# Kernel tuning notes

Measured on AMD Instinct MI355X. Metric: run time of the kernel, lower is better.

Reference implementation:

```python
import jax, jax.numpy as jnp
import numpy as np

D_MODEL = 1024
N_HEADS = 16
DK = D_MODEL // N_HEADS


def setup_inputs() -> dict:
    key = jax.random.key(0)
    k1, k2, k3, k4 = jax.random.split(key, 4)
    x = jax.random.normal(k1, (2, 2048, D_MODEL), dtype=jnp.float32)
    # torch nn.Linear stores weight as [out_features, in_features]
    W_qkv = jax.random.normal(k2, (3 * D_MODEL, D_MODEL), dtype=jnp.float32) * (1.0 / np.sqrt(D_MODEL))
    W_proj = jax.random.normal(k3, (D_MODEL, D_MODEL), dtype=jnp.float32) * (1.0 / np.sqrt(D_MODEL))
    b_proj = jax.random.normal(k4, (D_MODEL,), dtype=jnp.float32) * 0.01
    return {"x": x, "W_qkv": W_qkv, "W_proj": W_proj, "b_proj": b_proj}


def reference(x, W_qkv, W_proj, b_proj):
    B, L, D = x.shape
    qkv = x @ W_qkv.T                      # [B, L, 3D]
    q, k, v = jnp.split(qkv, 3, axis=-1)   # each [B, L, D]

    def split_heads(t):
        return t.reshape(B, L, N_HEADS, DK).transpose(0, 2, 1, 3)  # [B, H, L, dk]

    q, k, v = map(split_heads, (q, k, v))
    scale = jnp.float32(1.0 / np.sqrt(DK))
    scores = jnp.einsum('bhid,bhjd->bhij', q, k) * scale  # [B, H, L, L]
    attn = jax.nn.softmax(scores, axis=-1)
    out = jnp.einsum('bhij,bhjd->bhid', attn, v)           # [B, H, L, dk]
    out = out.transpose(0, 2, 1, 3).reshape(B, L, D)
    return out @ W_proj.T + b_proj
```

## Files before the change

kernel.cpp:

```cpp
#include <hip/hip_runtime.h>
#include <stdint.h>

typedef unsigned short ushort_t;
typedef __bf16 bf16x4 __attribute__((ext_vector_type(4)));
typedef __bf16 bf16x8 __attribute__((ext_vector_type(8)));
typedef float f32x4 __attribute__((ext_vector_type(4)));
typedef float f32x16 __attribute__((ext_vector_type(16)));
typedef unsigned short us8 __attribute__((ext_vector_type(8)));
typedef unsigned short us4v __attribute__((ext_vector_type(4)));

__device__ __forceinline__ float bf2f(ushort_t u) {
  union { uint32_t u; float f; } v; v.u = ((uint32_t)u) << 16; return v.f;
}
__device__ __forceinline__ ushort_t f2bf(float f) {
  union { float f; uint32_t u; } v; v.f = f;
  uint32_t u = v.u;
  uint32_t r = (u + 0x7FFFu + ((u >> 16) & 1u)) >> 16;
  return (ushort_t)r;
}
__device__ __forceinline__ uint32_t pkbf(float a, float b) {
  __bf16 x = (__bf16)a, y = (__bf16)b;
  uint32_t ux = __builtin_bit_cast(unsigned short, x);
  uint32_t uy = __builtin_bit_cast(unsigned short, y);
  return ux | (uy << 16);
}
__device__ __forceinline__ void gload_lds16(const void* g, void* l) {
  __builtin_amdgcn_global_load_lds(
      (const __attribute__((address_space(1))) void*)g,
      (__attribute__((address_space(3))) void*)l, 16, 0, 0);
}
__device__ __forceinline__ void tr2(const ushort_t* p, bf16x4& lo, bf16x4& hi) {
  asm volatile("ds_read_b64_tr_b16 %0, %2\n\t"
               "ds_read_b64_tr_b16 %1, %2 offset:128"
               : "=&v"(lo), "=&v"(hi)
               : "v"((const __attribute__((address_space(3))) ushort_t*)p));
}

template <typename T> __device__ __forceinline__ T to_out(float f);
template <> __device__ __forceinline__ ushort_t to_out<ushort_t>(float f) { return f2bf(f); }
template <> __device__ __forceinline__ float to_out<float>(float f) { return f; }

#define SCQ 0.1803368801111204f

__global__ void f2b3_kernel(const float* __restrict__ a, ushort_t* __restrict__ ao,
                            const float* __restrict__ b, ushort_t* __restrict__ bo,
                            const float* __restrict__ c, ushort_t* __restrict__ co) {
  int blk = blockIdx.x;
  const float* src; ushort_t* dst; int n4, b0, nb;
  if (blk < 1024)      { src = a; dst = ao; n4 = 1048576; b0 = blk;        nb = 1024; }
  else if (blk < 1792) { src = b; dst = bo; n4 = 786432;  b0 = blk - 1024; nb = 768; }
  else                 { src = c; dst = co; n4 = 262144;  b0 = blk - 1792; nb = 256; }
  for (int i = b0 * 256 + threadIdx.x; i < n4; i += nb * 256) {
    float4 v = ((const float4*)src)[i];
    us4v o;
    o[0] = f2bf(v.x); o[1] = f2bf(v.y); o[2] = f2bf(v.z); o[3] = f2bf(v.w);
    ((us4v*)dst)[i] = o;
  }
}

template<bool BIAS, typename OT, bool SCALEQ, bool MERGEA>
__global__ __launch_bounds__(256, 2) void gemm_bt(
    const ushort_t* __restrict__ A, const ushort_t* __restrict__ W,
    const float* __restrict__ bias, OT* __restrict__ C,
    int M, int N, int K,
    const ushort_t* __restrict__ A2, const float* __restrict__ lb)
{
  __shared__ ushort_t As[128 * 64];
  __shared__ ushort_t Bs[128 * 64];
  const int t = threadIdx.x;
  const int w = t >> 6, lane = t & 63;
  const int lg = lane >> 4, lc = lane & 15;
  const int rowbase = blockIdx.y * 128;
  const int colbase = blockIdx.x * 128;
  const int wr = (w >> 1) * 64, wc = (w & 1) * 64;

  f32x4 acc[4][4] = {};
  const int nkt = K >> 6;

  for (int kt = 0; kt < nkt; ++kt) {
#pragma unroll
    for (int i = 0; i < 4; ++i) {
      int off = (i * 256 + t) * 16;
      int row = off >> 7;
      int cb  = off & 127;
      int ec  = cb ^ ((row & 7) << 4);
      if constexpr (MERGEA) {
        int drow = rowbase + row;
        int kcol = kt * 64 + (cb >> 1);
        us8 v1 = *(const us8*)(A  + (size_t)drow * K + kcol);
        us8 v2 = *(const us8*)(A2 + (size_t)drow * K + kcol);
        float inv = 1.f / (lb[(size_t)drow * 16 + (kcol >> 6)] +
                           lb[65536 + (size_t)drow * 16 + (kcol >> 6)]);
        us8 o;
#pragma unroll
        for (int j = 0; j < 8; ++j)
          o[j] = f2bf((bf2f(v1[j]) + bf2f(v2[j])) * inv);
        *(us8*)((char*)As + (off ^ ((row & 7) << 4))) = o;
      } else {
        gload_lds16(A + (size_t)(rowbase + row) * K + kt * 64 + (ec >> 1),
                    (char*)As + off);
      }
      gload_lds16(W + (size_t)(colbase + row) * K + kt * 64 + (ec >> 1),
                  (char*)Bs + off);
    }
    __syncthreads();
#pragma unroll
    for (int kk = 0; kk < 2; ++kk) {
      bf16x8 af[4], bf[4];
#pragma unroll
      for (int m = 0; m < 4; ++m) {
        int row = wr + m * 16 + lc;
        int kb  = (lg * 16 + kk * 64) ^ ((row & 7) << 4);
        af[m] = *(const bf16x8*)((const char*)As + row * 128 + kb);
        int col = wc + m * 16 + lc;
        int kb2 = (lg * 16 + kk * 64) ^ ((col & 7) << 4);
        bf[m] = *(const bf16x8*)((const char*)Bs + col * 128 + kb2);
      }
#pragma unroll
      for (int m = 0; m < 4; ++m)
#pragma unroll
        for (int n = 0; n < 4; ++n)
          acc[m][n] = __builtin_amdgcn_mfma_f32_16x16x32_bf16(af[m], bf[n],
                                                              acc[m][n], 0, 0, 0);
    }
    __syncthreads();
  }

#pragma unroll
  for (int m = 0; m < 4; ++m) {
    int r0 = rowbase + wr + m * 16 + lg * 4;
#pragma unroll
    for (int n = 0; n < 4; ++n) {
      int c0 = colbase + wc + n * 16 + lc;
      float bv = 0.f;
      if (BIAS) bv = bias[c0];
      float qs = 1.f;
      if (SCALEQ) qs = (c0 < 1024) ? SCQ : 1.f;
#pragma unroll
      for (int j = 0; j < 4; ++j)
        C[(size_t)(r0 + j) * N + c0] = to_out<OT>(acc[m][n][j] * qs + bv);
    }
  }
}

__global__ __launch_bounds__(512, 4) void attn_fwd(
    const ushort_t* __restrict__ qkv, ushort_t* __restrict__ o1,
    ushort_t* __restrict__ o2, float* __restrict__ lbuf)
{
  __shared__ ushort_t Ks[2][64 * 64];
  __shared__ ushort_t Vs[2][64 * 64];

  const int t = threadIdx.x, w = t >> 6, lane = t & 63;
  const int l31 = lane & 31, hi = lane >> 5;
  const int lc = lane & 15;

  const int d = blockIdx.x;
  const int qt = (d >> 3) & 7;
  const int bhs = (d & 7) * 8 + (d >> 6);
  const int bh = bhs >> 1, split = bhs & 1;
  const int b = bh >> 4, h = bh & 15;

  const ushort_t* Qg = qkv + (size_t)(b * 2048) * 3072 + h * 64;
  const ushort_t* Kg = Qg + 1024 + (size_t)split * 1024 * 3072;
  const ushort_t* Vg = Qg + 2048 + (size_t)split * 1024 * 3072;

  auto stage_k = [&](ushort_t* Kd, int kt) {
    int off = t * 16;
    int row = off >> 7;
    int cb  = off & 127;
    int ec  = cb ^ ((row & 7) << 4);
    gload_lds16(Kg + (size_t)(kt * 64 + row) * 3072 + (ec >> 1),
                (char*)Kd + off);
  };
  const int vr  = t >> 3;
  const int vc0 = (t & 7) * 8;
  const int vdst = (vc0 >> 4) * 2048 + (vr >> 2) * 128 + (vr & 3) * 32 +
                   (vc0 & 8) * 2;

  const ushort_t* qrow_p = Qg + (size_t)(qt * 256 + w * 32 + l31) * 3072;
  bf16x8 qf[4];
#pragma unroll
  for (int kk = 0; kk < 4; ++kk)
    qf[kk] = *(const bf16x8*)(qrow_p + kk * 16 + hi * 8);

  stage_k(Ks[0], 0);
  {
    us8 v = *(const us8*)(Vg + (size_t)vr * 3072 + vc0);
    *(us8*)((char*)Vs[0] + vdst) = v;
  }
  __syncthreads();

  f32x16 oacc0 = {}, oacc1 = {};
  float l = 0.f;
  const int m16 = (lane >> 4) & 1;

  int cur = 0;
  for (int kt = 0; kt < 16; ++kt) {
    us8 vnext;
    if (kt < 15) {
      stage_k(Ks[cur ^ 1], kt + 1);
      vnext = *(const us8*)(Vg + (size_t)((kt + 1) * 64 + vr) * 3072 + vc0);
    }

    const ushort_t* Kc = Ks[cur];
    f32x16 s0 = {}, s1 = {};
    __builtin_amdgcn_s_setprio(1);
#pragma unroll
    for (int kk = 0; kk < 4; ++kk) {
      int cbyte = (kk * 32 + hi * 16);
      int r0 = l31, r1 = 32 + l31;
      bf16x8 kf0 = *(const bf16x8*)((const char*)Kc + r0 * 128 +
                                    (cbyte ^ ((r0 & 7) << 4)));
      bf16x8 kf1 = *(const bf16x8*)((const char*)Kc + r1 * 128 +
                                    (cbyte ^ ((r1 & 7) << 4)));
      s0 = __builtin_amdgcn_mfma_f32_32x32x16_bf16(kf0, qf[kk], s0, 0, 0, 0);
      s1 = __builtin_amdgcn_mfma_f32_32x32x16_bf16(kf1, qf[kk], s1, 0, 0, 0);
    }
    __builtin_amdgcn_s_setprio(0);

#pragma unroll
    for (int i = 0; i < 16; ++i) {
      s0[i] = __builtin_amdgcn_exp2f(s0[i]);
      s1[i] = __builtin_amdgcn_exp2f(s1[i]);
    }
    float rs = (((s0[0] + s0[1]) + (s0[2] + s0[3])) +
                ((s0[4] + s0[5]) + (s0[6] + s0[7]))) +
               (((s0[8] + s0[9]) + (s0[10] + s0[11])) +
                ((s0[12] + s0[13]) + (s0[14] + s0[15])));
    float rt = (((s1[0] + s1[1]) + (s1[2] + s1[3])) +
                ((s1[4] + s1[5]) + (s1[6] + s1[7]))) +
               (((s1[8] + s1[9]) + (s1[10] + s1[11])) +
                ((s1[12] + s1[13]) + (s1[14] + s1[15])));
    l += rs + rt;

    uint32_t pk0[8], pk1[8];
#pragma unroll
    for (int j = 0; j < 8; ++j) {
      pk0[j] = pkbf(s0[2 * j], s0[2 * j + 1]);
      pk1[j] = pkbf(s1[2 * j], s1[2 * j + 1]);
    }

    if (kt < 15)
      *(us8*)((char*)Vs[cur ^ 1] + vdst) = vnext;

    const ushort_t* Vc = Vs[cur];
    bf16x8 pa[4], vf[4][2];
#pragma unroll
    for (int ks = 0; ks < 4; ++ks) {
      int j0 = 4 * (ks & 1);
      uint32_t x0 = (ks < 2) ? pk0[j0]     : pk1[j0];
      uint32_t x1 = (ks < 2) ? pk0[j0 + 1] : pk1[j0 + 1];
      uint32_t y0 = (ks < 2) ? pk0[j0 + 2] : pk1[j0 + 2];
      uint32_t y1 = (ks < 2) ? pk0[j0 + 3] : pk1[j0 + 3];
      asm volatile("v_permlane32_swap_b32 %0, %1" : "+v"(x0), "+v"(y0));
      asm volatile("v_permlane32_swap_b32 %0, %1" : "+v"(x1), "+v"(y1));
      union { uint32_t du[4]; bf16x8 v; } U;
      U.du[0] = x0; U.du[1] = x1; U.du[2] = y0; U.du[3] = y1;
      pa[ks] = U.v;
#pragma unroll
      for (int nd = 0; nd < 2; ++nd) {
        bf16x4 lo, hh;
        tr2(Vc + (nd * 2 + m16) * 1024 + (4 * ks + 2 * hi) * 64 + lc * 4, lo, hh);
        vf[ks][nd] = __builtin_shufflevector(lo, hh, 0, 1, 2, 3, 4, 5, 6, 7);
      }
    }
    asm volatile("s_waitcnt lgkmcnt(0)" ::: "memory");
    __builtin_amdgcn_sched_barrier(0);
    __builtin_amdgcn_s_setprio(1);
#pragma unroll
    for (int ks = 0; ks < 4; ++ks) {
      oacc0 = __builtin_amdgcn_mfma_f32_32x32x16_bf16(pa[ks], vf[ks][0], oacc0, 0, 0, 0);
      oacc1 = __builtin_amdgcn_mfma_f32_32x32x16_bf16(pa[ks], vf[ks][1], oacc1, 0, 0, 0);
    }
    __builtin_amdgcn_s_setprio(0);

    __syncthreads();
    cur ^= 1;
  }

  l += __shfl_xor(l, 32);

  ushort_t* op = split ? o2 : o1;
#pragma unroll
  for (int r = 0; r < 16; ++r) {
    int crow = (r & 3) + 8 * (r >> 2) + 4 * hi;
    int qrow = qt * 256 + w * 32 + crow;
    size_t base = ((size_t)(b * 2048 + qrow)) * 1024 + h * 64 + l31;
    op[base]      = f2bf(oacc0[r]);
    op[base + 32] = f2bf(oacc1[r]);
  }
  if (hi == 0) {
    int qrow = qt * 256 + w * 32 + l31;
    lbuf[(size_t)split * 65536 + (size_t)(b * 2048 + qrow) * 16 + h] = l;
  }
}

extern "C" void kernel_launch(void* const* d_in, const int* in_sizes, int n_in,
                              void* d_out, int out_size, void* d_ws, size_t ws_size,
                              hipStream_t stream) {
  const float* x     = (const float*)d_in[0];
  const float* Wqkv  = (const float*)d_in[1];
  const float* Wproj = (const float*)d_in[2];
  const float* bproj = (const float*)d_in[3];
  float* out = (float*)d_out;

  ushort_t* qkv   = (ushort_t*)d_ws;
  ushort_t* o1    = qkv   + (size_t)4096 * 3072;
  ushort_t* xb    = o1    + (size_t)4096 * 1024;
  ushort_t* wqb   = xb    + (size_t)4096 * 1024;
  ushort_t* wpb   = wqb   + (size_t)3072 * 1024;
  float*    lbuf  = (float*)(wpb + (size_t)1024 * 1024);

  dim3 blk(256);
  f2b3_kernel<<<2048, blk, 0, stream>>>(x, xb, Wqkv, wqb, Wproj, wpb);

  gemm_bt<false, ushort_t, true, false><<<dim3(24, 32), blk, 0, stream>>>(
      xb, wqb, nullptr, qkv, 4096, 3072, 1024, nullptr, nullptr);
  attn_fwd<<<dim3(512), dim3(512), 0, stream>>>(qkv, o1, xb, lbuf);
  gemm_bt<true, float, false, true><<<dim3(8, 32), blk, 0, stream>>>(
      o1, wpb, bproj, out, 4096, 1024, 1024, xb, lbuf);
}
```

Baseline: 134.7 us.

## Split attention merge into separate kernel and remap GEMM blocks by XCD

The split-KV merge (sum of two partial outputs scaled by inverse softmax denominators) moves out of the projection GEMM's A-tile load into a standalone elementwise kernel. The projection GEMM can then use the async global-to-LDS load path again instead of synchronous vector loads plus arithmetic. Both GEMMs now use a 1D grid with a block-id remap that groups consecutive tiles onto the same XCD (id = (o&7)*(nwg/8) + o/8), aiming for better L2 locality. The cost is an extra kernel launch and an extra read/write pass over the 4096x1024 bf16 output.

```diff
diff --git a/kernel.cpp b/kernel.cpp
--- a/kernel.cpp
+++ b/kernel.cpp
@@ -58,20 +58,24 @@
   }
 }
 
-template<bool BIAS, typename OT, bool SCALEQ, bool MERGEA>
+template<bool BIAS, typename OT, bool SCALEQ>
 __global__ __launch_bounds__(256, 2) void gemm_bt(
     const ushort_t* __restrict__ A, const ushort_t* __restrict__ W,
     const float* __restrict__ bias, OT* __restrict__ C,
-    int M, int N, int K,
-    const ushort_t* __restrict__ A2, const float* __restrict__ lb)
+    int M, int N, int K)
 {
   __shared__ ushort_t As[128 * 64];
   __shared__ ushort_t Bs[128 * 64];
   const int t = threadIdx.x;
   const int w = t >> 6, lane = t & 63;
   const int lg = lane >> 4, lc = lane & 15;
-  const int rowbase = blockIdx.y * 128;
-  const int colbase = blockIdx.x * 128;
+
+  const int NX = N >> 7;
+  const int nwg = gridDim.x;
+  const int o = blockIdx.x;
+  const int id = (o & 7) * (nwg >> 3) + (o >> 3);
+  const int rowbase = (id / NX) * 128;
+  const int colbase = (id % NX) * 128;
   const int wr = (w >> 1) * 64, wc = (w & 1) * 64;
 
   f32x4 acc[4][4] = {};
@@ -84,22 +88,8 @@
       int row = off >> 7;
       int cb  = off & 127;
       int ec  = cb ^ ((row & 7) << 4);
-      if constexpr (MERGEA) {
-        int drow = rowbase + row;
-        int kcol = kt * 64 + (cb >> 1);
-        us8 v1 = *(const us8*)(A  + (size_t)drow * K + kcol);
-        us8 v2 = *(const us8*)(A2 + (size_t)drow * K + kcol);
-        float inv = 1.f / (lb[(size_t)drow * 16 + (kcol >> 6)] +
-                           lb[65536 + (size_t)drow * 16 + (kcol >> 6)]);
-        us8 o;
-#pragma unroll
-        for (int j = 0; j < 8; ++j)
-          o[j] = f2bf((bf2f(v1[j]) + bf2f(v2[j])) * inv);
-        *(us8*)((char*)As + (off ^ ((row & 7) << 4))) = o;
-      } else {
-        gload_lds16(A + (size_t)(rowbase + row) * K + kt * 64 + (ec >> 1),
-                    (char*)As + off);
-      }
+      gload_lds16(A + (size_t)(rowbase + row) * K + kt * 64 + (ec >> 1),
+                  (char*)As + off);
       gload_lds16(W + (size_t)(colbase + row) * K + kt * 64 + (ec >> 1),
                   (char*)Bs + off);
     }
@@ -295,6 +285,25 @@
   }
 }
 
+__global__ void merge_kernel(ushort_t* __restrict__ o1,
+                             const ushort_t* __restrict__ o2,
+                             const float* __restrict__ lbuf) {
+  int i = blockIdx.x * blockDim.x + threadIdx.x;
+  int row = i >> 7;
+  int col = (i & 127) * 8;
+  int h = col >> 6;
+  float l1 = lbuf[(size_t)row * 16 + h];
+  float l2 = lbuf[65536 + (size_t)row * 16 + h];
+  float inv = 1.f / (l1 + l2);
+  us8 v1 = ((const us8*)o1)[i];
+  us8 v2 = ((const us8*)o2)[i];
+  us8 o;
+#pragma unroll
+  for (int j = 0; j < 8; ++j)
+    o[j] = f2bf((bf2f(v1[j]) + bf2f(v2[j])) * inv);
+  ((us8*)o1)[i] = o;
+}
+
 extern "C" void kernel_launch(void* const* d_in, const int* in_sizes, int n_in,
                               void* d_out, int out_size, void* d_ws, size_t ws_size,
                               hipStream_t stream) {
@@ -314,9 +323,10 @@
   dim3 blk(256);
   f2b3_kernel<<<2048, blk, 0, stream>>>(x, xb, Wqkv, wqb, Wproj, wpb);
 
-  gemm_bt<false, ushort_t, true, false><<<dim3(24, 32), blk, 0, stream>>>(
-      xb, wqb, nullptr, qkv, 4096, 3072, 1024, nullptr, nullptr);
+  gemm_bt<false, ushort_t, true><<<768, blk, 0, stream>>>(
+      xb, wqb, nullptr, qkv, 4096, 3072, 1024);
   attn_fwd<<<dim3(512), dim3(512), 0, stream>>>(qkv, o1, xb, lbuf);
-  gemm_bt<true, float, false, true><<<dim3(8, 32), blk, 0, stream>>>(
-      o1, wpb, bproj, out, 4096, 1024, 1024, xb, lbuf);
-}
+  merge_kernel<<<2048, blk, 0, stream>>>(o1, xb, lbuf);
+  gemm_bt<true, float, false><<<256, blk, 0, stream>>>(
+      o1, wpb, bproj, out, 4096, 1024, 1024);
+}
```

After: 111.1 us. -17.5%, faster.
